# Kernel tuning notes

Hardware: AMD Instinct MI355X
Metric: run time of the kernel (lower is better)

The kernel has to match this reference:

```python
import jax, jax.numpy as jnp
import numpy as np

HIDDEN = 768
NUM_BLOCKS = 8
BLOCK = HIDDEN // NUM_BLOCKS
BASE_THR, K_DECAY, MIN_THR = 0.01, 20.0, 0.0005


def _threshold(height, width):
    # wavenumber-dependent soft-shrink threshold T(k), shape [H, W//2+1]
    fu = jnp.fft.fftfreq(height, d=1.0).astype(jnp.float32)[:, None]
    fv = jnp.fft.rfftfreq(width, d=1.0).astype(jnp.float32)[None, :]
    k = jnp.sqrt(fu ** 2 + fv ** 2) * max(height, width)
    thr = BASE_THR * jnp.exp(-0.5 * (k / K_DECAY) ** 2)
    return jnp.maximum(thr, MIN_THR)


def setup_inputs() -> dict:
    key = jax.random.key(0)
    kx, k1, k2, k3, k4 = jax.random.split(key, 5)
    scale = 0.02
    x = jax.random.normal(kx, (4, 128, 128, HIDDEN), dtype=jnp.float32)
    w1 = scale * jax.random.normal(k1, (2, NUM_BLOCKS, BLOCK, BLOCK), dtype=jnp.float32)
    b1 = scale * jax.random.normal(k2, (2, NUM_BLOCKS, BLOCK), dtype=jnp.float32)
    w2 = scale * jax.random.normal(k3, (2, NUM_BLOCKS, BLOCK, BLOCK), dtype=jnp.float32)
    b2 = scale * jax.random.normal(k4, (2, NUM_BLOCKS, BLOCK), dtype=jnp.float32)
    return {"x": x, "w1": w1, "b1": b1, "w2": w2, "b2": b2}


def reference(x, w1, b1, w2, b2):
    dtype = x.dtype
    bias = x
    xf = x.astype(jnp.float32)
    B, H, W, C = xf.shape
    Wc = W // 2 + 1
    # rfft2 over spatial dims, orthonormal
    Xc = jnp.fft.rfft2(xf, axes=(1, 2), norm='ortho')
    Xc = Xc.reshape(B, H, Wc, NUM_BLOCKS, BLOCK)
    xr, xi = jnp.real(Xc), jnp.imag(Xc)
    mm = lambda t, w: jnp.einsum('bhwni,nio->bhwno', t, w)
    # complex block-diagonal 2-layer MLP
    o1r = jax.nn.relu(mm(xr, w1[0]) - mm(xi, w1[1]) + b1[0])
    o1i = jax.nn.relu(mm(xi, w1[0]) + mm(xr, w1[1]) + b1[1])
    o2r = mm(o1r, w2[0]) - mm(o1i, w2[1]) + b2[0]
    o2i = mm(o1i, w2[0]) + mm(o1r, w2[1]) + b2[1]
    # soft-shrink on complex magnitude with wavenumber-dependent threshold
    mag = jnp.sqrt(o2r ** 2 + o2i ** 2 + 1e-8)
    thr = _threshold(H, W)[None, :, :, None, None]  # [1,H,Wc,1,1]
    sf = jax.nn.relu(mag - thr) / mag
    Yc = (o2r * sf) + 1j * (o2i * sf)
    Yc = Yc.reshape(B, H, Wc, C)
    y = jnp.fft.irfft2(Yc, s=(H, W), axes=(1, 2), norm='ortho')
    return y.astype(dtype) + bias
```

## Files before the change

### kernel.cpp

```cpp
#include <hip/hip_runtime.h>
#include <hip/hip_bf16.h>
#include <math.h>


#define HD   768
#define NBLK 8
#define HH   128
#define WW   128
#define WC   65
#define NPOS (HH * WC)

constexpr float SC    = 0.08838834764831845f;
constexpr float TWOPI = 6.28318530717958647692f;

constexpr int TM_OFF     = 0;
constexpr int TW_OFF     = 131072;
constexpr int TWI_OFF    = 151552;
constexpr int WF_OFF     = 172032;
constexpr int WF_END_U16 = 466944;
constexpr size_t A_UINTS = (size_t)4 * NPOS * HD;

typedef __attribute__((ext_vector_type(8))) short short8;
typedef __attribute__((ext_vector_type(4))) float f32x4;

#define MFMA __builtin_amdgcn_mfma_f32_16x16x32_bf16

static __device__ inline unsigned short f2bf(float f) {
  __hip_bfloat16 h = __float2bfloat16(f);
  return __builtin_bit_cast(unsigned short, h);
}
static __device__ inline unsigned int pack2(float re, float im) {
  return (unsigned int)f2bf(re) | ((unsigned int)f2bf(im) << 16);
}
static __device__ inline short8 lo8(uint4 a, uint4 b) {
  uint4 r = { (a.x & 0xffffu) | (a.y << 16), (a.z & 0xffffu) | (a.w << 16),
              (b.x & 0xffffu) | (b.y << 16), (b.z & 0xffffu) | (b.w << 16) };
  return __builtin_bit_cast(short8, r);
}
static __device__ inline short8 hi8(uint4 a, uint4 b) {
  uint4 r = { (a.x >> 16) | (a.y & 0xffff0000u), (a.z >> 16) | (a.w & 0xffff0000u),
              (b.x >> 16) | (b.y & 0xffff0000u), (b.z >> 16) | (b.w & 0xffff0000u) };
  return __builtin_bit_cast(short8, r);
}

__global__ __launch_bounds__(256) void k_prep(const float* __restrict__ w1,
                                              const float* __restrict__ b1,
                                              const float* __restrict__ w2,
                                              const float* __restrict__ b2,
                                              unsigned short* __restrict__ wf,
                                              float* __restrict__ bpk) {
  const int blk = blockIdx.x, t = threadIdx.x;
  if (blk < 16) {
    const int layer = blk >> 3, n = blk & 7;
    const float* w  = layer ? w2 : w1;
    const float* bs = layer ? b2 : b1;
    unsigned short* dst = wf + WF_OFF + (size_t)blk * (36 * 512);
    for (int e = t; e < 36 * 512; e += 256) {
      int f = e >> 9, idx = e & 511;
      int kk = f / 12, nt = f - kk * 12;
      int lane = idx >> 3, j = idx & 7;
      int k = kk * 32 + (lane >> 4) * 8 + j;
      int cc = nt * 16 + (lane & 15);
      float v = (cc < 96) ? w[(size_t)n * 9216 + k * 96 + cc]
                          : w[(size_t)(8 + n) * 9216 + k * 96 + (cc - 96)];
      dst[e] = f2bf(v);
    }
    for (int c = t; c < 192; c += 256)
      bpk[blk * 192 + c] = (c < 96) ? bs[n * 96 + c] : bs[(8 + n) * 96 + (c - 96)];
  } else if (blk < 18) {
    const int base = (blk - 16) * 128;
    for (int e = t; e < 128 * 512; e += 256) {
      int f = base + (e >> 9), idx = e & 511;
      int dir = f >> 7, part = (f >> 6) & 1, kot = (f >> 3) & 7, kk = f & 7;
      int lane = idx >> 3, j = idx & 7;
      int ko = kot * 16 + (lane & 15);
      int k  = kk * 32 + (lane >> 4) * 8 + j;
      int r  = k & 127;
      float sn, cs; sincosf((TWOPI / 128.f) * (float)((ko * r) & 127), &sn, &cs);
      float v;
      if (dir == 0) v = part ? (k < 128 ? -sn : cs) : (k < 128 ? cs : sn);
      else          v = part ? (k < 128 ?  sn : cs) : (k < 128 ? cs : -sn);
      wf[TM_OFF + (size_t)f * 512 + idx] = f2bf(v * SC);
    }
  } else if (blk == 18) {
    for (int e = t; e < 40 * 512; e += 256) {
      int f = e >> 9, idx = e & 511;
      int mt = f >> 2, kk = f & 3;
      int lane = idx >> 3, j = idx & 7;
      int row = mt * 16 + (lane & 15);
      int r   = kk * 32 + (lane >> 4) * 8 + j;
      int kor = (row < 80) ? row : row - 80;
      float sn, cs; sincosf((TWOPI / 128.f) * (float)((kor * r) & 127), &sn, &cs);
      wf[TW_OFF + (size_t)f * 512 + idx] = f2bf((row < 80 ? cs : -sn) * SC);
    }
  } else {
    for (int e = t; e < 40 * 512; e += 256) {
      int f = e >> 9, idx = e & 511;
      int mt = f / 5, kk = f - mt * 5;
      int lane = idx >> 3, j = idx & 7;
      int wr = mt * 16 + (lane & 15);
      int k  = kk * 32 + (lane >> 4) * 8 + j;
      float v = 0.f;
      if (k < 80) {
        int kb = k;
        if (kb <= 64) {
          float sn, cs; sincosf((TWOPI / 128.f) * (float)((wr * kb) & 127), &sn, &cs);
          v = SC * ((kb == 0 || kb == 64) ? 1.f : 2.f) * cs;
        }
      } else {
        int kb = k - 80;
        if (kb >= 1 && kb <= 63) {
          float sn, cs; sincosf((TWOPI / 128.f) * (float)((wr * kb) & 127), &sn, &cs);
          v = -2.f * SC * sn;
        }
      }
      wf[TWI_OFF + (size_t)f * 512 + idx] = f2bf(v);
    }
  }
}

__global__ __launch_bounds__(256) void k_fft_w(const float* __restrict__ x,
                                               unsigned int* __restrict__ A,
                                               const unsigned short* __restrict__ wf) {
  __shared__ unsigned short Xt[64 * 136];
  const int h = blockIdx.x, c0 = blockIdx.y * 64, b = blockIdx.z, t = threadIdx.x;
  const int wv = t >> 6, lane = t & 63, l15 = lane & 15, lg = lane >> 4;
  const float* xp = x + ((size_t)(b * HH + h)) * WW * HD + c0;
  for (int idx = t; idx < 128 * 64; idx += 256) {
    int r = idx >> 6, ch = idx & 63;
    Xt[ch * 136 + r] = f2bf(xp[(size_t)r * HD + ch]);
  }
  __syncthreads();
  const unsigned short* tw = wf + TW_OFF;
  f32x4 acc[10];
#pragma unroll
  for (int m = 0; m < 10; ++m) acc[m] = { 0.f, 0.f, 0.f, 0.f };
#pragma unroll
  for (int kk = 0; kk < 4; ++kk) {
    short8 bq = *(const short8*)&Xt[(wv * 16 + l15) * 136 + kk * 32 + lg * 8];
#pragma unroll
    for (int m = 0; m < 10; ++m) {
      short8 a = *(const short8*)&tw[(size_t)(m * 4 + kk) * 512 + lane * 8];
      acc[m] = MFMA(a, bq, acc[m], 0, 0, 0);
    }
  }
  unsigned int* Ao = A + ((size_t)b * NPOS + h * WC) * HD + c0 + wv * 16 + l15;
#pragma unroll
  for (int q = 0; q < 5; ++q)
#pragma unroll
    for (int r = 0; r < 4; ++r) {
      int ko = q * 16 + lg * 4 + r;
      if (ko <= 64) Ao[(size_t)ko * HD] = pack2(acc[q][r], acc[5 + q][r]);
    }
}

__global__ __launch_bounds__(256) void k_ifft_w(const unsigned int* __restrict__ A,
                                                const float* __restrict__ x,
                                                float* __restrict__ out,
                                                const unsigned short* __restrict__ wf) {
  __shared__ unsigned short Zt[64 * 168];
  const int h = blockIdx.x, c0 = blockIdx.y * 64, b = blockIdx.z, t = threadIdx.x;
  const int wv = t >> 6, lane = t & 63, l15 = lane & 15, lg = lane >> 4;
  const unsigned int* Ai = A + ((size_t)b * NPOS + h * WC) * HD + c0;
  for (int idx = t; idx < 65 * 64; idx += 256) {
    int kb = idx >> 6, ch = idx & 63;
    unsigned int u = Ai[(size_t)kb * HD + ch];
    Zt[ch * 168 + kb]      = (unsigned short)(u & 0xffffu);
    Zt[ch * 168 + 80 + kb] = (unsigned short)(u >> 16);
  }
  for (int idx = t; idx < 64 * 32; idx += 256) {
    int ch = idx >> 5, q = idx & 31;
    if (q < 30) {
      int kb = 65 + (q % 15), half = q / 15;
      Zt[ch * 168 + half * 80 + kb] = 0;
    }
  }
  __syncthreads();
  const unsigned short* twi = wf + TWI_OFF;
  f32x4 acc[8];
#pragma unroll
  for (int m = 0; m < 8; ++m) acc[m] = { 0.f, 0.f, 0.f, 0.f };
#pragma unroll
  for (int kk = 0; kk < 5; ++kk) {
    short8 bq = *(const short8*)&Zt[(wv * 16 + l15) * 168 + kk * 32 + lg * 8];
#pragma unroll
    for (int m = 0; m < 8; ++m) {
      short8 a = *(const short8*)&twi[(size_t)(m * 5 + kk) * 512 + lane * 8];
      acc[m] = MFMA(a, bq, acc[m], 0, 0, 0);
    }
  }
#pragma unroll
  for (int m = 0; m < 8; ++m)
#pragma unroll
    for (int r = 0; r < 4; ++r) {
      int wr = m * 16 + lg * 4 + r;
      size_t go = (((size_t)(b * HH + h)) * WW + wr) * HD + c0 + wv * 16 + l15;
      out[go] = acc[m][r] + x[go];
    }
}

#define ZCS 132
#define ZQS 100

static __device__ inline short8 afragq(const unsigned int* Zq, int row, int k0) {
  const unsigned int* z = Zq + row * ZQS + (k0 < 96 ? k0 : k0 - 96);
  uint4 a = *(const uint4*)z, b = *(const uint4*)(z + 4);
  return (k0 < 96) ? lo8(a, b) : hi8(a, b);
}

template <int DIRBASE>
static __device__ inline void dft_gemm(const unsigned int* Zc, const unsigned short* tm,
                                       int w, int lane, f32x4* aR, f32x4* aI) {
  const int l15 = lane & 15, lg = lane >> 4;
#pragma unroll
  for (int kkr = 0; kkr < 4; ++kkr) {
    const int r0 = kkr * 32 + lg * 8;
    short8 aRlo = *(const short8*)&tm[(size_t)(DIRBASE + w * 8 + kkr) * 512 + lane * 8];
    short8 aRhi = *(const short8*)&tm[(size_t)(DIRBASE + w * 8 + kkr + 4) * 512 + lane * 8];
    short8 aIlo = *(const short8*)&tm[(size_t)(DIRBASE + 64 + w * 8 + kkr) * 512 + lane * 8];
    short8 aIhi = *(const short8*)&tm[(size_t)(DIRBASE + 64 + w * 8 + kkr + 4) * 512 + lane * 8];
#pragma unroll
    for (int co = 0; co < 6; ++co) {
      const unsigned int* z = Zc + (co * 16 + l15) * ZCS + r0;
      uint4 za = *(const uint4*)z;
      uint4 zb = *(const uint4*)(z + 4);
      short8 blo = lo8(za, zb);
      short8 bhi = hi8(za, zb);
      aR[co] = MFMA(aRlo, blo, aR[co], 0, 0, 0);
      aR[co] = MFMA(aRhi, bhi, aR[co], 0, 0, 0);
      aI[co] = MFMA(aIlo, blo, aI[co], 0, 0, 0);
      aI[co] = MFMA(aIhi, bhi, aI[co], 0, 0, 0);
    }
  }
}

__global__ __launch_bounds__(512) void k_mid(unsigned int* __restrict__ A,
                                             const unsigned short* __restrict__ wf,
                                             const float* __restrict__ bpk) {
  __shared__ unsigned int Zb[12800];
  __shared__ unsigned short WfL[36 * 512];
  const int kv = blockIdx.x, n = blockIdx.y, b = blockIdx.z, t = threadIdx.x;
  const int wid = t >> 6, lane = t & 63, l15 = lane & 15, lg = lane >> 4;
  unsigned int* Abase = A + ((size_t)b * NPOS + kv) * HD + n * 96;
  const unsigned short* tm = wf + TM_OFF;

  for (int idx = t; idx < 128 * 96; idx += 512) {
    int r = idx / 96, ch = idx - r * 96;
    Zb[ch * ZCS + r] = Abase[(size_t)r * (WC * HD) + ch];
  }
  {
    const int4* src = (const int4*)(wf + WF_OFF + (size_t)n * (36 * 512));
    for (int idx = t; idx < 2304; idx += 512) ((int4*)WfL)[idx] = src[idx];
  }
  __syncthreads();

  f32x4 aR[6], aI[6];
#pragma unroll
  for (int co = 0; co < 6; ++co) { aR[co] = {0.f,0.f,0.f,0.f}; aI[co] = {0.f,0.f,0.f,0.f}; }
  dft_gemm<0>(Zb, tm, wid, lane, aR, aI);
  __syncthreads();
#pragma unroll
  for (int co = 0; co < 6; ++co)
#pragma unroll
    for (int r = 0; r < 4; ++r)
      Zb[(wid * 16 + lg * 4 + r) * ZQS + co * 16 + l15] = pack2(aR[co][r], aI[co][r]);
  __syncthreads();

  f32x4 acc[12];
#pragma unroll
  for (int nt = 0; nt < 12; ++nt) {
    float bv = bpk[n * 192 + nt * 16 + l15];
    acc[nt] = { bv, bv, bv, bv };
  }
#pragma unroll
  for (int kk = 0; kk < 6; ++kk) {
    short8 a = afragq(Zb, wid * 16 + l15, kk * 32 + lg * 8);
#pragma unroll
    for (int nt = 0; nt < 12; ++nt) {
      short8 bfr;
      if (kk < 3) bfr = *(const short8*)&WfL[(kk * 12 + nt) * 512 + lane * 8];
      else {
        int nt2 = (nt < 6) ? nt + 6 : nt - 6;
        int4 nb = *(const int4*)&WfL[((kk - 3) * 12 + nt2) * 512 + lane * 8];
        if (nt < 6) { nb.x ^= 0x80008000; nb.y ^= 0x80008000; nb.z ^= 0x80008000; nb.w ^= 0x80008000; }
        bfr = __builtin_bit_cast(short8, nb);
      }
      acc[nt] = MFMA(a, bfr, acc[nt], 0, 0, 0);
    }
  }
#pragma unroll
  for (int nt = 0; nt < 6; ++nt)
#pragma unroll
    for (int r = 0; r < 4; ++r)
      Zb[(wid * 16 + lg * 4 + r) * ZQS + nt * 16 + l15] =
          pack2(fmaxf(acc[nt][r], 0.f), fmaxf(acc[nt + 6][r], 0.f));
  __syncthreads();
  {
    const int4* src = (const int4*)(wf + WF_OFF + (size_t)(8 + n) * (36 * 512));
    for (int idx = t; idx < 2304; idx += 512) ((int4*)WfL)[idx] = src[idx];
  }
#pragma unroll
  for (int nt = 0; nt < 12; ++nt) {
    float bv = bpk[(8 + n) * 192 + nt * 16 + l15];
    acc[nt] = { bv, bv, bv, bv };
  }
  __syncthreads();

#pragma unroll
  for (int kk = 0; kk < 6; ++kk) {
    short8 a = afragq(Zb, wid * 16 + l15, kk * 32 + lg * 8);
#pragma unroll
    for (int nt = 0; nt < 12; ++nt) {
      short8 bfr;
      if (kk < 3) bfr = *(const short8*)&WfL[(kk * 12 + nt) * 512 + lane * 8];
      else {
        int nt2 = (nt < 6) ? nt + 6 : nt - 6;
        int4 nb = *(const int4*)&WfL[((kk - 3) * 12 + nt2) * 512 + lane * 8];
        if (nt < 6) { nb.x ^= 0x80008000; nb.y ^= 0x80008000; nb.z ^= 0x80008000; nb.w ^= 0x80008000; }
        bfr = __builtin_bit_cast(short8, nb);
      }
      acc[nt] = MFMA(a, bfr, acc[nt], 0, 0, 0);
    }
  }
  __syncthreads();

#pragma unroll
  for (int r = 0; r < 4; ++r) {
    int ko = wid * 16 + lg * 4 + r;
    float kus = (ko >= 64) ? (float)(ko - 128) : (float)ko;
    float k2v = kus * kus + (float)(kv * kv);
    float thr = fmaxf(0.01f * expf(-0.00125f * k2v), 0.0005f);
#pragma unroll
    for (int nt = 0; nt < 6; ++nt) {
      float mr = acc[nt][r], mi = acc[nt + 6][r];
      float mag = sqrtf(mr * mr + mi * mi + 1e-8f);
      float sf = fmaxf(mag - thr, 0.f) / mag;
      Zb[(nt * 16 + l15) * ZCS + ko] = pack2(mr * sf, mi * sf);
    }
  }
  __syncthreads();

#pragma unroll
  for (int co = 0; co < 6; ++co) { aR[co] = {0.f,0.f,0.f,0.f}; aI[co] = {0.f,0.f,0.f,0.f}; }
  dft_gemm<128>(Zb, tm, wid, lane, aR, aI);
#pragma unroll
  for (int co = 0; co < 6; ++co)
#pragma unroll
    for (int r = 0; r < 4; ++r) {
      int rr = wid * 16 + lg * 4 + r;
      Abase[(size_t)rr * (WC * HD) + co * 16 + l15] = pack2(aR[co][r], aI[co][r]);
    }
}

extern "C" void kernel_launch(void* const* d_in, const int* in_sizes, int n_in,
                              void* d_out, int out_size, void* d_ws, size_t ws_size,
                              hipStream_t stream) {
  const float* x  = (const float*)d_in[0];
  const float* w1 = (const float*)d_in[1];
  const float* b1 = (const float*)d_in[2];
  const float* w2 = (const float*)d_in[3];
  const float* b2 = (const float*)d_in[4];
  float* out = (float*)d_out;
  unsigned int* A = (unsigned int*)d_ws;

  unsigned short* wf = (unsigned short*)(A + A_UINTS);
  float* bpk = (float*)(wf + WF_END_U16);

  k_prep<<<20, 256, 0, stream>>>(w1, b1, w2, b2, wf, bpk);
  k_fft_w<<<dim3(HH, HD / 64, 4), 256, 0, stream>>>(x, A, wf);
  k_mid<<<dim3(WC, NBLK, 4), 512, 0, stream>>>(A, wf, bpk);
  k_ifft_w<<<dim3(HH, HD / 64, 4), 256, 0, stream>>>(A, x, out, wf);
}
```

Before: 454.3 us.

## Split LDS into real/imag planes, compact DFT tables, stream MLP weights from global

The middle kernel now keeps the spectrum in separate real and imaginary bf16 planes in LDS. This lets the DFT GEMM use three shared cos/sin/-sin matrices for both directions instead of separate per-direction lo/hi tables, shrinking the twiddle table. MLP weights are pre-expanded into a full complex block matrix in the prep kernel and read straight from global/L2. That removes the LDS weight staging, the sign-flip XOR work and several barriers. Shared memory per block drops substantially, which may raise occupancy, at the cost of more global/L2 weight traffic inside the GEMM loops.

```diff
diff --git a/kernel.cpp b/kernel.cpp
--- a/kernel.cpp
+++ b/kernel.cpp
@@ -14,10 +14,10 @@
 constexpr float TWOPI = 6.28318530717958647692f;
 
 constexpr int TM_OFF     = 0;
-constexpr int TW_OFF     = 131072;
-constexpr int TWI_OFF    = 151552;
-constexpr int WF_OFF     = 172032;
-constexpr int WF_END_U16 = 466944;
+constexpr int TW_OFF     = 49152;
+constexpr int TWI_OFF    = 69632;
+constexpr int WF_OFF     = 90112;
+constexpr int WF_END_U16 = 679936;
 constexpr size_t A_UINTS = (size_t)4 * NPOS * HD;
 
 typedef __attribute__((ext_vector_type(8))) short short8;
@@ -54,35 +54,34 @@
     const int layer = blk >> 3, n = blk & 7;
     const float* w  = layer ? w2 : w1;
     const float* bs = layer ? b2 : b1;
-    unsigned short* dst = wf + WF_OFF + (size_t)blk * (36 * 512);
-    for (int e = t; e < 36 * 512; e += 256) {
+    unsigned short* dst = wf + WF_OFF + (size_t)blk * (72 * 512);
+    for (int e = t; e < 72 * 512; e += 256) {
       int f = e >> 9, idx = e & 511;
       int kk = f / 12, nt = f - kk * 12;
       int lane = idx >> 3, j = idx & 7;
-      int k = kk * 32 + (lane >> 4) * 8 + j;
+      int k  = kk * 32 + (lane >> 4) * 8 + j;
       int cc = nt * 16 + (lane & 15);
-      float v = (cc < 96) ? w[(size_t)n * 9216 + k * 96 + cc]
-                          : w[(size_t)(8 + n) * 9216 + k * 96 + (cc - 96)];
+      float v;
+      if (k < 96) v = (cc < 96) ? w[(size_t)n * 9216 + k * 96 + cc]
+                                : w[(size_t)(8 + n) * 9216 + k * 96 + (cc - 96)];
+      else        v = (cc < 96) ? -w[(size_t)(8 + n) * 9216 + (k - 96) * 96 + cc]
+                                :  w[(size_t)n * 9216 + (k - 96) * 96 + (cc - 96)];
       dst[e] = f2bf(v);
     }
     for (int c = t; c < 192; c += 256)
       bpk[blk * 192 + c] = (c < 96) ? bs[n * 96 + c] : bs[(8 + n) * 96 + (c - 96)];
-  } else if (blk < 18) {
-    const int base = (blk - 16) * 128;
-    for (int e = t; e < 128 * 512; e += 256) {
-      int f = base + (e >> 9), idx = e & 511;
-      int dir = f >> 7, part = (f >> 6) & 1, kot = (f >> 3) & 7, kk = f & 7;
+  } else if (blk == 16) {
+    for (int e = t; e < 96 * 512; e += 256) {
+      int f = e >> 9, idx = e & 511;
+      int part = f >> 5, rem = f & 31, kot = rem >> 2, kk = rem & 3;
       int lane = idx >> 3, j = idx & 7;
       int ko = kot * 16 + (lane & 15);
-      int k  = kk * 32 + (lane >> 4) * 8 + j;
-      int r  = k & 127;
+      int r  = kk * 32 + (lane >> 4) * 8 + j;
       float sn, cs; sincosf((TWOPI / 128.f) * (float)((ko * r) & 127), &sn, &cs);
-      float v;
-      if (dir == 0) v = part ? (k < 128 ? -sn : cs) : (k < 128 ? cs : sn);
-      else          v = part ? (k < 128 ?  sn : cs) : (k < 128 ? cs : -sn);
+      float v = (part == 0) ? cs : (part == 1) ? sn : -sn;
       wf[TM_OFF + (size_t)f * 512 + idx] = f2bf(v * SC);
     }
-  } else if (blk == 18) {
+  } else if (blk == 17) {
     for (int e = t; e < 40 * 512; e += 256) {
       int f = e >> 9, idx = e & 511;
       int mt = f >> 2, kk = f & 3;
@@ -199,37 +198,38 @@
     }
 }
 
-#define ZCS 132
-#define ZQS 100
-
 static __device__ inline short8 afragq(const unsigned int* Zq, int row, int k0) {
-  const unsigned int* z = Zq + row * ZQS + (k0 < 96 ? k0 : k0 - 96);
+  const unsigned int* z = Zq + row * 100 + (k0 < 96 ? k0 : k0 - 96);
   uint4 a = *(const uint4*)z, b = *(const uint4*)(z + 4);
   return (k0 < 96) ? lo8(a, b) : hi8(a, b);
 }
 
-template <int DIRBASE>
-static __device__ inline void dft_gemm(const unsigned int* Zc, const unsigned short* tm,
-                                       int w, int lane, f32x4* aR, f32x4* aI) {
+template <int FWD>
+static __device__ inline void dft_gemm(const unsigned short* Rb, const unsigned short* Ib,
+                                       const unsigned short* tm, int w, int lane,
+                                       f32x4* aR, f32x4* aI) {
   const int l15 = lane & 15, lg = lane >> 4;
 #pragma unroll
   for (int kkr = 0; kkr < 4; ++kkr) {
     const int r0 = kkr * 32 + lg * 8;
-    short8 aRlo = *(const short8*)&tm[(size_t)(DIRBASE + w * 8 + kkr) * 512 + lane * 8];
-    short8 aRhi = *(const short8*)&tm[(size_t)(DIRBASE + w * 8 + kkr + 4) * 512 + lane * 8];
-    short8 aIlo = *(const short8*)&tm[(size_t)(DIRBASE + 64 + w * 8 + kkr) * 512 + lane * 8];
-    short8 aIhi = *(const short8*)&tm[(size_t)(DIRBASE + 64 + w * 8 + kkr + 4) * 512 + lane * 8];
+    short8 Ac = *(const short8*)&tm[(size_t)(0 * 32 + w * 4 + kkr) * 512 + lane * 8];
+    short8 As = *(const short8*)&tm[(size_t)(1 * 32 + w * 4 + kkr) * 512 + lane * 8];
+    short8 An = *(const short8*)&tm[(size_t)(2 * 32 + w * 4 + kkr) * 512 + lane * 8];
 #pragma unroll
     for (int co = 0; co < 6; ++co) {
-      const unsigned int* z = Zc + (co * 16 + l15) * ZCS + r0;
-      uint4 za = *(const uint4*)z;
-      uint4 zb = *(const uint4*)(z + 4);
-      short8 blo = lo8(za, zb);
-      short8 bhi = hi8(za, zb);
-      aR[co] = MFMA(aRlo, blo, aR[co], 0, 0, 0);
-      aR[co] = MFMA(aRhi, bhi, aR[co], 0, 0, 0);
-      aI[co] = MFMA(aIlo, blo, aI[co], 0, 0, 0);
-      aI[co] = MFMA(aIhi, bhi, aI[co], 0, 0, 0);
+      short8 zr = *(const short8*)&Rb[(co * 16 + l15) * 136 + r0];
+      short8 zi = *(const short8*)&Ib[(co * 16 + l15) * 136 + r0];
+      if constexpr (FWD) {
+        aR[co] = MFMA(Ac, zr, aR[co], 0, 0, 0);
+        aR[co] = MFMA(As, zi, aR[co], 0, 0, 0);
+        aI[co] = MFMA(Ac, zi, aI[co], 0, 0, 0);
+        aI[co] = MFMA(An, zr, aI[co], 0, 0, 0);
+      } else {
+        aR[co] = MFMA(Ac, zr, aR[co], 0, 0, 0);
+        aR[co] = MFMA(An, zi, aR[co], 0, 0, 0);
+        aI[co] = MFMA(Ac, zi, aI[co], 0, 0, 0);
+        aI[co] = MFMA(As, zr, aI[co], 0, 0, 0);
+      }
     }
   }
 }
@@ -237,8 +237,11 @@
 __global__ __launch_bounds__(512) void k_mid(unsigned int* __restrict__ A,
                                              const unsigned short* __restrict__ wf,
                                              const float* __restrict__ bpk) {
-  __shared__ unsigned int Zb[12800];
-  __shared__ unsigned short WfL[36 * 512];
+  __shared__ unsigned short Ub[2 * 13312];
+  unsigned short* Rb = Ub;
+  unsigned short* Ib = Ub + 13312;
+  unsigned int* Zq = (unsigned int*)Ub;
+
   const int kv = blockIdx.x, n = blockIdx.y, b = blockIdx.z, t = threadIdx.x;
   const int wid = t >> 6, lane = t & 63, l15 = lane & 15, lg = lane >> 4;
   unsigned int* Abase = A + ((size_t)b * NPOS + kv) * HD + n * 96;
@@ -246,26 +249,25 @@
 
   for (int idx = t; idx < 128 * 96; idx += 512) {
     int r = idx / 96, ch = idx - r * 96;
-    Zb[ch * ZCS + r] = Abase[(size_t)r * (WC * HD) + ch];
-  }
-  {
-    const int4* src = (const int4*)(wf + WF_OFF + (size_t)n * (36 * 512));
-    for (int idx = t; idx < 2304; idx += 512) ((int4*)WfL)[idx] = src[idx];
+    unsigned int u = Abase[(size_t)r * (WC * HD) + ch];
+    Rb[ch * 136 + r] = (unsigned short)(u & 0xffffu);
+    Ib[ch * 136 + r] = (unsigned short)(u >> 16);
   }
   __syncthreads();
 
   f32x4 aR[6], aI[6];
 #pragma unroll
   for (int co = 0; co < 6; ++co) { aR[co] = {0.f,0.f,0.f,0.f}; aI[co] = {0.f,0.f,0.f,0.f}; }
-  dft_gemm<0>(Zb, tm, wid, lane, aR, aI);
+  dft_gemm<1>(Rb, Ib, tm, wid, lane, aR, aI);
   __syncthreads();
 #pragma unroll
   for (int co = 0; co < 6; ++co)
 #pragma unroll
     for (int r = 0; r < 4; ++r)
-      Zb[(wid * 16 + lg * 4 + r) * ZQS + co * 16 + l15] = pack2(aR[co][r], aI[co][r]);
-  __syncthreads();
-
+      Zq[(wid * 16 + lg * 4 + r) * 100 + co * 16 + l15] = pack2(aR[co][r], aI[co][r]);
+
+  const unsigned short* wf1 = wf + WF_OFF + (size_t)n * (72 * 512);
+  const unsigned short* wf2 = wf + WF_OFF + (size_t)(8 + n) * (72 * 512);
   f32x4 acc[12];
 #pragma unroll
   for (int nt = 0; nt < 12; ++nt) {
@@ -274,17 +276,10 @@
   }
 #pragma unroll
   for (int kk = 0; kk < 6; ++kk) {
-    short8 a = afragq(Zb, wid * 16 + l15, kk * 32 + lg * 8);
+    short8 a = afragq(Zq, wid * 16 + l15, kk * 32 + lg * 8);
 #pragma unroll
     for (int nt = 0; nt < 12; ++nt) {
-      short8 bfr;
-      if (kk < 3) bfr = *(const short8*)&WfL[(kk * 12 + nt) * 512 + lane * 8];
-      else {
-        int nt2 = (nt < 6) ? nt + 6 : nt - 6;
-        int4 nb = *(const int4*)&WfL[((kk - 3) * 12 + nt2) * 512 + lane * 8];
-        if (nt < 6) { nb.x ^= 0x80008000; nb.y ^= 0x80008000; nb.z ^= 0x80008000; nb.w ^= 0x80008000; }
-        bfr = __builtin_bit_cast(short8, nb);
-      }
+      short8 bfr = *(const short8*)&wf1[(size_t)(kk * 12 + nt) * 512 + lane * 8];
       acc[nt] = MFMA(a, bfr, acc[nt], 0, 0, 0);
     }
   }
@@ -292,33 +287,20 @@
   for (int nt = 0; nt < 6; ++nt)
 #pragma unroll
     for (int r = 0; r < 4; ++r)
-      Zb[(wid * 16 + lg * 4 + r) * ZQS + nt * 16 + l15] =
+      Zq[(wid * 16 + lg * 4 + r) * 100 + nt * 16 + l15] =
           pack2(fmaxf(acc[nt][r], 0.f), fmaxf(acc[nt + 6][r], 0.f));
-  __syncthreads();
-  {
-    const int4* src = (const int4*)(wf + WF_OFF + (size_t)(8 + n) * (36 * 512));
-    for (int idx = t; idx < 2304; idx += 512) ((int4*)WfL)[idx] = src[idx];
-  }
+
 #pragma unroll
   for (int nt = 0; nt < 12; ++nt) {
     float bv = bpk[(8 + n) * 192 + nt * 16 + l15];
     acc[nt] = { bv, bv, bv, bv };
   }
-  __syncthreads();
-
 #pragma unroll
   for (int kk = 0; kk < 6; ++kk) {
-    short8 a = afragq(Zb, wid * 16 + l15, kk * 32 + lg * 8);
+    short8 a = afragq(Zq, wid * 16 + l15, kk * 32 + lg * 8);
 #pragma unroll
     for (int nt = 0; nt < 12; ++nt) {
-      short8 bfr;
-      if (kk < 3) bfr = *(const short8*)&WfL[(kk * 12 + nt) * 512 + lane * 8];
-      else {
-        int nt2 = (nt < 6) ? nt + 6 : nt - 6;
-        int4 nb = *(const int4*)&WfL[((kk - 3) * 12 + nt2) * 512 + lane * 8];
-        if (nt < 6) { nb.x ^= 0x80008000; nb.y ^= 0x80008000; nb.z ^= 0x80008000; nb.w ^= 0x80008000; }
-        bfr = __builtin_bit_cast(short8, nb);
-      }
+      short8 bfr = *(const short8*)&wf2[(size_t)(kk * 12 + nt) * 512 + lane * 8];
       acc[nt] = MFMA(a, bfr, acc[nt], 0, 0, 0);
     }
   }
@@ -335,14 +317,15 @@
       float mr = acc[nt][r], mi = acc[nt + 6][r];
       float mag = sqrtf(mr * mr + mi * mi + 1e-8f);
       float sf = fmaxf(mag - thr, 0.f) / mag;
-      Zb[(nt * 16 + l15) * ZCS + ko] = pack2(mr * sf, mi * sf);
+      Rb[(nt * 16 + l15) * 136 + ko] = f2bf(mr * sf);
+      Ib[(nt * 16 + l15) * 136 + ko] = f2bf(mi * sf);
     }
   }
   __syncthreads();
 
 #pragma unroll
   for (int co = 0; co < 6; ++co) { aR[co] = {0.f,0.f,0.f,0.f}; aI[co] = {0.f,0.f,0.f,0.f}; }
-  dft_gemm<128>(Zb, tm, wid, lane, aR, aI);
+  dft_gemm<0>(Rb, Ib, tm, wid, lane, aR, aI);
 #pragma unroll
   for (int co = 0; co < 6; ++co)
 #pragma unroll
@@ -366,7 +349,7 @@
   unsigned short* wf = (unsigned short*)(A + A_UINTS);
   float* bpk = (float*)(wf + WF_END_U16);
 
-  k_prep<<<20, 256, 0, stream>>>(w1, b1, w2, b2, wf, bpk);
+  k_prep<<<19, 256, 0, stream>>>(w1, b1, w2, b2, wf, bpk);
   k_fft_w<<<dim3(HH, HD / 64, 4), 256, 0, stream>>>(x, A, wf);
   k_mid<<<dim3(WC, NBLK, 4), 512, 0, stream>>>(A, wf, bpk);
   k_ifft_w<<<dim3(HH, HD / 64, 4), 256, 0, stream>>>(A, x, out, wf);
```

New measurement: 625.0 us. 37.6% more time.
